# Kernel optimization log

Measured on AMD Instinct MI355X. Metric: run time of the kernel, lower is better.

## Reference

```python
import jax, jax.numpy as jnp
import numpy as np

V_TH = 1.0
V_RESET = 0.0
ALPHA = 4.0  # sigmoid surrogate sharpness used by the Triton backward kernel


@jax.custom_vjp
def spike_fn(over_th):
    # Heaviside forward; sigmoid surrogate gradient in backward.
    return (over_th >= 0).astype(over_th.dtype)


def _spike_fwd(over_th):
    return spike_fn(over_th), over_th


def _spike_bwd(over_th, g):
    sig = jax.nn.sigmoid(ALPHA * over_th)
    return (g * (1.0 - sig) * sig * ALPHA,)


spike_fn.defvjp(_spike_fwd, _spike_bwd)


def setup_inputs() -> dict:
    key = jax.random.key(0)
    k1, _ = jax.random.split(key)
    T, B, D = 32, 128, 8192
    x_seq = jax.random.normal(k1, (T, B, D), dtype=jnp.float32)
    v_init = jnp.zeros((B, D), dtype=jnp.float32)  # module init: v = v_reset = 0.0
    return {"x_seq": x_seq, "v_init": v_init}


def reference(x_seq, v_init):
    # IF neuron, multi-step, hard reset:
    #   h_t   = x_t + v_{t-1}
    #   s_t   = H(h_t - v_th)
    #   v_t   = h_t * (1 - s_t) + v_reset * s_t
    def step(v, x):
        h = x + v
        s = spike_fn(h - V_TH)
        v_next = h * (1.0 - s) + V_RESET * s
        return v_next, s

    _, spike_seq = jax.lax.scan(step, v_init, x_seq)
    return spike_seq
```

## Files before the change

### kernel.cpp

```cpp
#include <hip/hip_runtime.h>


typedef float v2f __attribute__((ext_vector_type(2)));

template <int T, int KB>
__global__ __launch_bounds__(256) void if_node_pipe_barrier(
    const float* __restrict__ x,
    const float* __restrict__ v0,
    float* __restrict__ out,
    long n2)
{
    long i = (long)blockIdx.x * blockDim.x + threadIdx.x;
    if (i >= n2) return;

    const v2f* __restrict__ x2 = (const v2f*)x;
    v2f*       __restrict__ o2 = (v2f*)out;

    v2f v = ((const v2f*)v0)[i];

    constexpr int G = T / KB;
    v2f buf[2][KB];

#pragma unroll
    for (int k = 0; k < KB; ++k)
        buf[0][k] = x2[(long)k * n2 + i];
    __builtin_amdgcn_sched_barrier(0);

#pragma unroll
    for (int g = 0; g < G; ++g) {
        const int cb = g & 1;
        if (g + 1 < G) {
#pragma unroll
            for (int k = 0; k < KB; ++k)
                buf[cb ^ 1][k] = x2[(long)((g + 1) * KB + k) * n2 + i];
            __builtin_amdgcn_sched_barrier(0);
        }
#pragma unroll
        for (int k = 0; k < KB; ++k) {
            float hx = buf[cb][k].x + v.x;
            float hy = buf[cb][k].y + v.y;
            bool sx = (hx - 1.0f) >= 0.0f;
            bool sy = (hy - 1.0f) >= 0.0f;
            v2f s;
            s.x = sx ? 1.0f : 0.0f;
            s.y = sy ? 1.0f : 0.0f;
            v.x = sx ? 0.0f : hx;
            v.y = sy ? 0.0f : hy;
            __builtin_nontemporal_store(s, &o2[(long)(g * KB + k) * n2 + i]);
        }
        __builtin_amdgcn_sched_barrier(0);
    }
}

__global__ __launch_bounds__(256) void if_node_f2_generic(
    const float* __restrict__ x, const float* __restrict__ v0,
    float* __restrict__ out, long n2, int T)
{
    long i = (long)blockIdx.x * blockDim.x + threadIdx.x;
    if (i >= n2) return;
    const v2f* x2 = (const v2f*)x;
    v2f*       o2 = (v2f*)out;
    v2f v = ((const v2f*)v0)[i];
    for (int t = 0; t < T; ++t) {
        v2f xv = x2[(long)t * n2 + i];
        float hx = xv.x + v.x;
        float hy = xv.y + v.y;
        bool sx = (hx - 1.0f) >= 0.0f;
        bool sy = (hy - 1.0f) >= 0.0f;
        v2f s;
        s.x = sx ? 1.0f : 0.0f;
        s.y = sy ? 1.0f : 0.0f;
        v.x = sx ? 0.0f : hx;
        v.y = sy ? 0.0f : hy;
        o2[(long)t * n2 + i] = s;
    }
}

__global__ __launch_bounds__(256) void if_node_scalar(
    const float* __restrict__ x, const float* __restrict__ v0,
    float* __restrict__ out, long n, int T)
{
    long i = (long)blockIdx.x * blockDim.x + threadIdx.x;
    if (i >= n) return;
    float v = v0[i];
    for (int t = 0; t < T; ++t) {
        float h = x[(long)t * n + i] + v;
        bool s = (h - 1.0f) >= 0.0f;
        out[(long)t * n + i] = s ? 1.0f : 0.0f;
        v = s ? 0.0f : h;
    }
}

extern "C" void kernel_launch(void* const* d_in, const int* in_sizes, int n_in,
                              void* d_out, int out_size, void* d_ws, size_t ws_size,
                              hipStream_t stream) {
    const float* x  = (const float*)d_in[0];
    const float* v0 = (const float*)d_in[1];
    float* out = (float*)d_out;

    long n = in_sizes[1];
    int  T = (int)(in_sizes[0] / n);

    int block = 256;
    if (T == 32 && (n & 1) == 0) {
        long n2 = n >> 1;
        long grid = (n2 + block - 1) / block;
        if_node_pipe_barrier<32, 8><<<dim3((unsigned)grid), dim3(block), 0, stream>>>(
            x, v0, out, n2);
    } else if ((n & 1) == 0) {
        long n2 = n >> 1;
        long grid = (n2 + block - 1) / block;
        if_node_f2_generic<<<dim3((unsigned)grid), dim3(block), 0, stream>>>(
            x, v0, out, n2, T);
    } else {
        long grid = (n + block - 1) / block;
        if_node_scalar<<<dim3((unsigned)grid), dim3(block), 0, stream>>>(
            x, v0, out, n, T);
    }
}
```

Measured before the change: 237.9 us.

## Process multiple strided columns per thread and drop explicit double-buffer pipeline

Replaces the double-buffered time-chunk pipeline with a kernel where each thread handles C=4 independent float2 columns strided by q, loading all C columns per timestep and fully unrolling over T. This trades per-thread temporal prefetching for independent column parallelism, exposing more in-flight loads through independent recurrences instead of sched_barrier-based prefetch. It cuts the grid to a quarter and raises per-thread register use, which may reduce occupancy and latency hiding.

```diff
diff --git a/kernel.cpp b/kernel.cpp
--- a/kernel.cpp
+++ b/kernel.cpp
@@ -3,52 +3,46 @@
 
 typedef float v2f __attribute__((ext_vector_type(2)));
 
-template <int T, int KB>
-__global__ __launch_bounds__(256) void if_node_pipe_barrier(
+template <int T, int C>
+__global__ __launch_bounds__(256) void if_node_multicol(
     const float* __restrict__ x,
     const float* __restrict__ v0,
     float* __restrict__ out,
-    long n2)
+    long q)
 {
     long i = (long)blockIdx.x * blockDim.x + threadIdx.x;
-    if (i >= n2) return;
+    if (i >= q) return;
 
     const v2f* __restrict__ x2 = (const v2f*)x;
     v2f*       __restrict__ o2 = (v2f*)out;
+    const v2f* __restrict__ vv = (const v2f*)v0;
 
-    v2f v = ((const v2f*)v0)[i];
+    const long n2 = q * C;
 
-    constexpr int G = T / KB;
-    v2f buf[2][KB];
+    v2f v[C];
+#pragma unroll
+    for (int c = 0; c < C; ++c)
+        v[c] = vv[i + (long)c * q];
 
 #pragma unroll
-    for (int k = 0; k < KB; ++k)
-        buf[0][k] = x2[(long)k * n2 + i];
-    __builtin_amdgcn_sched_barrier(0);
-
+    for (int t = 0; t < T; ++t) {
+        v2f xv[C];
 #pragma unroll
-    for (int g = 0; g < G; ++g) {
-        const int cb = g & 1;
-        if (g + 1 < G) {
+        for (int c = 0; c < C; ++c)
+            xv[c] = x2[(long)t * n2 + i + (long)c * q];
 #pragma unroll
-            for (int k = 0; k < KB; ++k)
-                buf[cb ^ 1][k] = x2[(long)((g + 1) * KB + k) * n2 + i];
-            __builtin_amdgcn_sched_barrier(0);
-        }
-#pragma unroll
-        for (int k = 0; k < KB; ++k) {
-            float hx = buf[cb][k].x + v.x;
-            float hy = buf[cb][k].y + v.y;
+        for (int c = 0; c < C; ++c) {
+            float hx = xv[c].x + v[c].x;
+            float hy = xv[c].y + v[c].y;
             bool sx = (hx - 1.0f) >= 0.0f;
             bool sy = (hy - 1.0f) >= 0.0f;
             v2f s;
             s.x = sx ? 1.0f : 0.0f;
             s.y = sy ? 1.0f : 0.0f;
-            v.x = sx ? 0.0f : hx;
-            v.y = sy ? 0.0f : hy;
-            __builtin_nontemporal_store(s, &o2[(long)(g * KB + k) * n2 + i]);
+            v[c].x = sx ? 0.0f : hx;
+            v[c].y = sy ? 0.0f : hy;
+            __builtin_nontemporal_store(s, &o2[(long)t * n2 + i + (long)c * q]);
         }
-        __builtin_amdgcn_sched_barrier(0);
     }
 }
 
@@ -102,11 +96,13 @@
     int  T = (int)(in_sizes[0] / n);
 
     int block = 256;
-    if (T == 32 && (n & 1) == 0) {
+    constexpr int C = 4;
+    if (T == 32 && (n % (2 * C)) == 0) {
         long n2 = n >> 1;
-        long grid = (n2 + block - 1) / block;
-        if_node_pipe_barrier<32, 8><<<dim3((unsigned)grid), dim3(block), 0, stream>>>(
-            x, v0, out, n2);
+        long q  = n2 / C;
+        long grid = (q + block - 1) / block;
+        if_node_multicol<32, C><<<dim3((unsigned)grid), dim3(block), 0, stream>>>(
+            x, v0, out, q);
     } else if ((n & 1) == 0) {
         long n2 = n >> 1;
         long grid = (n2 + block - 1) / block;
```

New measurement: 230.9 us. 2.9% less time.

## Split IF neuron into bitmask compute pass and parallel float expand pass

Applied to the files above, without the earlier changes.

The scan kernel now reads x as float4, packs each element's 32 spike bits into one 32-bit mask in workspace, and does no float output stores. A second kernel with a grid dimension over time expands the masks into float spikes with fully parallel nontemporal stores. This takes the large output write out of the serial time loop so it can run with full parallelism, at the cost of a second launch, a small workspace round trip, and fewer threads in the compute pass. It falls back to the old path if the workspace is too small.

```diff
diff --git a/kernel.cpp b/kernel.cpp
--- a/kernel.cpp
+++ b/kernel.cpp
@@ -1,55 +1,89 @@
 #include <hip/hip_runtime.h>
 
 
-typedef float v2f __attribute__((ext_vector_type(2)));
+typedef float    v4f __attribute__((ext_vector_type(4)));
+typedef unsigned v4u __attribute__((ext_vector_type(4)));
+typedef float    v2f __attribute__((ext_vector_type(2)));
 
-template <int T, int KB>
-__global__ __launch_bounds__(256) void if_node_pipe_barrier(
+template <int T>
+__global__ __launch_bounds__(256) void if_bitmask_compute(
     const float* __restrict__ x,
     const float* __restrict__ v0,
-    float* __restrict__ out,
-    long n2)
+    unsigned* __restrict__ masks,
+    long n4)
 {
-    long i = (long)blockIdx.x * blockDim.x + threadIdx.x;
-    if (i >= n2) return;
+    static_assert(T % 8 == 0 && T <= 32, "");
+    long g = (long)blockIdx.x * blockDim.x + threadIdx.x;
+    if (g >= n4) return;
 
-    const v2f* __restrict__ x2 = (const v2f*)x;
-    v2f*       __restrict__ o2 = (v2f*)out;
+    const v4f* __restrict__ x4 = (const v4f*)x;
+    v4f v = ((const v4f*)v0)[g];
 
-    v2f v = ((const v2f*)v0)[i];
+    unsigned m0 = 0u, m1 = 0u, m2 = 0u, m3 = 0u;
 
-    constexpr int G = T / KB;
-    v2f buf[2][KB];
-
+    v4f cur[8], nxt[8];
 #pragma unroll
-    for (int k = 0; k < KB; ++k)
-        buf[0][k] = x2[(long)k * n2 + i];
+    for (int k = 0; k < 8; ++k)
+        cur[k] = x4[(long)k * n4 + g];
     __builtin_amdgcn_sched_barrier(0);
 
 #pragma unroll
-    for (int g = 0; g < G; ++g) {
-        const int cb = g & 1;
-        if (g + 1 < G) {
+    for (int gb = 0; gb < T / 8; ++gb) {
+        if (gb + 1 < T / 8) {
 #pragma unroll
-            for (int k = 0; k < KB; ++k)
-                buf[cb ^ 1][k] = x2[(long)((g + 1) * KB + k) * n2 + i];
-            __builtin_amdgcn_sched_barrier(0);
+            for (int k = 0; k < 8; ++k)
+                nxt[k] = x4[(long)((gb + 1) * 8 + k) * n4 + g];
         }
+        __builtin_amdgcn_sched_barrier(0);
 #pragma unroll
-        for (int k = 0; k < KB; ++k) {
-            float hx = buf[cb][k].x + v.x;
-            float hy = buf[cb][k].y + v.y;
-            bool sx = (hx - 1.0f) >= 0.0f;
-            bool sy = (hy - 1.0f) >= 0.0f;
-            v2f s;
-            s.x = sx ? 1.0f : 0.0f;
-            s.y = sy ? 1.0f : 0.0f;
-            v.x = sx ? 0.0f : hx;
-            v.y = sy ? 0.0f : hy;
-            __builtin_nontemporal_store(s, &o2[(long)(g * KB + k) * n2 + i]);
+        for (int k = 0; k < 8; ++k) {
+            const int t = gb * 8 + k;
+            float h0 = cur[k].x + v.x;
+            float h1 = cur[k].y + v.y;
+            float h2 = cur[k].z + v.z;
+            float h3 = cur[k].w + v.w;
+            bool s0 = (h0 - 1.0f) >= 0.0f;
+            bool s1 = (h1 - 1.0f) >= 0.0f;
+            bool s2 = (h2 - 1.0f) >= 0.0f;
+            bool s3 = (h3 - 1.0f) >= 0.0f;
+            m0 |= s0 ? (1u << t) : 0u;
+            m1 |= s1 ? (1u << t) : 0u;
+            m2 |= s2 ? (1u << t) : 0u;
+            m3 |= s3 ? (1u << t) : 0u;
+            v.x = s0 ? 0.0f : h0;
+            v.y = s1 ? 0.0f : h1;
+            v.z = s2 ? 0.0f : h2;
+            v.w = s3 ? 0.0f : h3;
+        }
+        if (gb + 1 < T / 8) {
+#pragma unroll
+            for (int k = 0; k < 8; ++k)
+                cur[k] = nxt[k];
         }
         __builtin_amdgcn_sched_barrier(0);
     }
+
+    v4u mm;
+    mm.x = m0; mm.y = m1; mm.z = m2; mm.w = m3;
+    __builtin_nontemporal_store(mm, &((v4u*)masks)[g]);
+}
+
+__global__ __launch_bounds__(256) void if_bitmask_expand(
+    const unsigned* __restrict__ masks,
+    float* __restrict__ out,
+    long n4)
+{
+    long g = (long)blockIdx.x * blockDim.x + threadIdx.x;
+    if (g >= n4) return;
+    const unsigned t = blockIdx.y;
+
+    v4u m = ((const v4u*)masks)[g];
+    v4f s;
+    s.x = ((m.x >> t) & 1u) ? 1.0f : 0.0f;
+    s.y = ((m.y >> t) & 1u) ? 1.0f : 0.0f;
+    s.z = ((m.z >> t) & 1u) ? 1.0f : 0.0f;
+    s.w = ((m.w >> t) & 1u) ? 1.0f : 0.0f;
+    __builtin_nontemporal_store(s, &((v4f*)out)[(long)t * n4 + g]);
 }
 
 __global__ __launch_bounds__(256) void if_node_f2_generic(
@@ -102,11 +136,17 @@
     int  T = (int)(in_sizes[0] / n);
 
     int block = 256;
-    if (T == 32 && (n & 1) == 0) {
-        long n2 = n >> 1;
-        long grid = (n2 + block - 1) / block;
-        if_node_pipe_barrier<32, 8><<<dim3((unsigned)grid), dim3(block), 0, stream>>>(
-            x, v0, out, n2);
+    bool fast = (T == 32) && ((n & 3) == 0) &&
+                (ws_size >= (size_t)n * sizeof(unsigned));
+
+    if (fast) {
+        long n4 = n >> 2;
+        unsigned* masks = (unsigned*)d_ws;
+        long grid = (n4 + block - 1) / block;
+        if_bitmask_compute<32><<<dim3((unsigned)grid), dim3(block), 0, stream>>>(
+            x, v0, masks, n4);
+        if_bitmask_expand<<<dim3((unsigned)grid, 32), dim3(block), 0, stream>>>(
+            masks, out, n4);
     } else if ((n & 1) == 0) {
         long n2 = n >> 1;
         long grid = (n2 + block - 1) / block;
```

Result: no change. 236.9 us (-0.4%).
